# Performance work log

Measured on AMD Instinct MI355X. Metric: run time of the kernel, lower is better.

Reference implementation:

```python
import jax, jax.numpy as jnp
import numpy as np

N = 100000   # nodes
E = 1000000  # edges
IN, HID, OUT = 128, 64, 64


def setup_inputs() -> dict:
    key = jax.random.key(0)
    ks = jax.random.split(key, 6)
    x = jax.random.normal(ks[0], (N, IN), dtype=jnp.float32)
    edge_index = jax.random.randint(ks[1], (2, E), 0, N, dtype=jnp.int64)
    edge_attr = jax.random.uniform(ks[2], (E,), dtype=jnp.float32)
    # Glorot-style init like PyG GCNConv (weight [in, out], bias zeros)
    W1 = jax.random.normal(ks[3], (IN, HID), dtype=jnp.float32) * (1.0 / np.sqrt(IN))
    b1 = jnp.zeros((HID,), dtype=jnp.float32)
    W2 = jax.random.normal(ks[4], (HID, OUT), dtype=jnp.float32) * (1.0 / np.sqrt(HID))
    b2 = jnp.zeros((OUT,), dtype=jnp.float32)
    return {"x": x, "edge_index": edge_index, "edge_attr": edge_attr,
            "W1": W1, "b1": b1, "W2": W2, "b2": b2}


def gcn_conv(x, edge_index, edge_weight, W, b):
    """GCNConv: add self-loops, symmetric normalization, linear + scatter-add."""
    n = x.shape[0]
    row, col = edge_index[0], edge_index[1]
    loop = jnp.arange(n, dtype=row.dtype)
    row = jnp.concatenate([row, loop])
    col = jnp.concatenate([col, loop])
    w = jnp.concatenate([edge_weight, jnp.ones((n,), dtype=x.dtype)])
    deg = jax.ops.segment_sum(w, col, num_segments=n)              # [N]
    dinv = jnp.where(deg > 0, jax.lax.rsqrt(deg), 0.0)
    norm = dinv[row] * w * dinv[col]                               # [E+N]
    h = x @ W                                                      # [N, out]
    agg = jax.ops.segment_sum(h[row] * norm[:, None], col, num_segments=n)
    return agg + b


def reference(x, edge_index, edge_attr, W1, b1, W2, b2):
    h = jax.nn.relu(gcn_conv(x, edge_index, edge_attr, W1, b1))
    return jax.nn.relu(gcn_conv(h, edge_index, edge_attr, W2, b2))
```

## Files before the change

### kernel.cpp

```cpp
#include <hip/hip_runtime.h>


#define BNODES 128
#define LB 7
#define MAXBKT 1024
#define EPT 16
#define EPB (256 * EPT)

typedef __attribute__((ext_vector_type(8))) short bf16x8;
typedef __attribute__((ext_vector_type(4))) float f32x4;

__device__ __forceinline__ unsigned short f2bf(float f) {
    unsigned u = __float_as_uint(f);
    u = (u + 0x7FFF + ((u >> 16) & 1)) >> 16;
    return (unsigned short)u;
}
__device__ __forceinline__ float bf2f(unsigned short h) {
    return __uint_as_float(((unsigned)h) << 16);
}

__device__ __forceinline__ int waveIncScan(int v, int lane) {
    #pragma unroll
    for (int d = 1; d < 64; d <<= 1) {
        int u = __shfl_up(v, d, 64);
        if (lane >= d) v += u;
    }
    return v;
}

__device__ __forceinline__ int blockIncScan(int v, int t, int* wt) {
    int lane = t & 63, w = t >> 6;
    int s = waveIncScan(v, lane);
    if (lane == 63) wt[w] = s;
    __syncthreads();
    int add = 0;
    #pragma unroll
    for (int i = 0; i < 3; ++i) if (i < w) add += wt[i];
    return s + add;
}

__device__ __forceinline__ float4 gather2(
    const unsigned short* __restrict__ G, const int2* __restrict__ eb,
    int m, int p, float4 a0)
{
    float4 a1 = make_float4(0.f, 0.f, 0.f, 0.f);
    int j = 0;
    for (; j + 1 < m; j += 2) {
        int2 pk0 = eb[j];
        int2 pk1 = eb[j + 1];
        float w0 = __int_as_float(pk0.y);
        float w1 = __int_as_float(pk1.y);
        ushort4 g0 = *(const ushort4*)&G[(size_t)pk0.x * 64 + p * 4];
        ushort4 g1 = *(const ushort4*)&G[(size_t)pk1.x * 64 + p * 4];
        a0.x = fmaf(w0, bf2f(g0.x), a0.x); a0.y = fmaf(w0, bf2f(g0.y), a0.y);
        a0.z = fmaf(w0, bf2f(g0.z), a0.z); a0.w = fmaf(w0, bf2f(g0.w), a0.w);
        a1.x = fmaf(w1, bf2f(g1.x), a1.x); a1.y = fmaf(w1, bf2f(g1.y), a1.y);
        a1.z = fmaf(w1, bf2f(g1.z), a1.z); a1.w = fmaf(w1, bf2f(g1.w), a1.w);
    }
    if (j < m) {
        int2 pk = eb[j];
        float w = __int_as_float(pk.y);
        ushort4 g = *(const ushort4*)&G[(size_t)pk.x * 64 + p * 4];
        a0.x = fmaf(w, bf2f(g.x), a0.x); a0.y = fmaf(w, bf2f(g.y), a0.y);
        a0.z = fmaf(w, bf2f(g.z), a0.z); a0.w = fmaf(w, bf2f(g.w), a0.w);
    }
    a0.x += a1.x; a0.y += a1.y; a0.z += a1.z; a0.w += a1.w;
    return a0;
}


__global__ __launch_bounds__(256) void hist_kernel(
    const int* __restrict__ col, int* __restrict__ H, int E, int NBKT,
    const float* __restrict__ W1, const float* __restrict__ W2,
    unsigned short* __restrict__ WT1, unsigned short* __restrict__ WT2, int NEB)
{
    int t = threadIdx.x, blk = blockIdx.x;
    if (blk >= NEB) {
        int i = (blk - NEB) * 256 + t;
        if (i < 64 * 128) {
            int c = i >> 7, k = i & 127;
            WT1[i] = f2bf(W1[k * 64 + c]);
        } else if (i < 64 * 128 + 64 * 64) {
            int j = i - 64 * 128;
            int c = j >> 6, k = j & 63;
            WT2[j] = f2bf(W2[k * 64 + c]);
        }
        return;
    }
    __shared__ int h[MAXBKT];
    for (int b = t; b < NBKT; b += 256) h[b] = 0;
    __syncthreads();
    int base = blk * EPB;
    #pragma unroll
    for (int i = 0; i < EPT; ++i) {
        int e = base + i * 256 + t;
        if (e < E) atomicAdd(&h[col[e] >> LB], 1);
    }
    __syncthreads();
    for (int b = t; b < NBKT; b += 256) H[blk * NBKT + b] = h[b];
}

__global__ __launch_bounds__(256) void rowscan_kernel(
    int* __restrict__ H, int* __restrict__ rowSum, int NEB, int NBKT)
{
    __shared__ int wt[4];
    int b = blockIdx.x, t = threadIdx.x;
    int v = (t < NEB) ? H[t * NBKT + b] : 0;
    int incl = blockIncScan(v, t, wt);
    if (t < NEB) H[t * NBKT + b] = incl - v;
    if (t == 255) rowSum[b] = incl;
}

__global__ __launch_bounds__(256) void bktscan_kernel(
    const int* __restrict__ rowSum, int* __restrict__ bktStart, int NBKT)
{
    __shared__ int wt[4];
    int t = threadIdx.x;
    int v[4]; int sum = 0;
    #pragma unroll
    for (int k = 0; k < 4; ++k) {
        int i = t * 4 + k;
        v[k] = (i < NBKT) ? rowSum[i] : 0;
        sum += v[k];
    }
    int incl = blockIncScan(sum, t, wt);
    int excl = incl - sum;
    #pragma unroll
    for (int k = 0; k < 4; ++k) {
        int i = t * 4 + k;
        if (i < NBKT) bktStart[i] = excl;
        excl += v[k];
    }
    if (t == 255) bktStart[NBKT] = incl;
}

__global__ __launch_bounds__(256) void scatter_gemm_kernel(
    const int* __restrict__ row, const int* __restrict__ col,
    const float* __restrict__ w, const int* __restrict__ H,
    const int* __restrict__ bktStart, int2* __restrict__ sedge1,
    int E, int NBKT, int NEB,
    const float* __restrict__ X, const unsigned short* __restrict__ WT,
    unsigned short* __restrict__ G, int n)
{
    __shared__ char smem[64 * 256 * 2];
    const int t = threadIdx.x;
    const int blk = blockIdx.x;

    if (blk < NEB) {
        int* cur = (int*)smem;
        for (int b = t; b < NBKT; b += 256) cur[b] = bktStart[b] + H[blk * NBKT + b];
        __syncthreads();
        int base = blk * EPB;
        #pragma unroll
        for (int i = 0; i < EPT; ++i) {
            int e = base + i * 256 + t;
            if (e < E) {
                int c = col[e];
                int b = c >> LB;
                int pos = atomicAdd(&cur[b], 1);
                int2 pk;
                pk.x = row[e] | ((c & (BNODES - 1)) << 20);
                pk.y = __float_as_int(w[e]);
                sedge1[pos] = pk;
            }
        }
        return;
    }

    constexpr int K = 128, ROWB = 256, SLOTS = 16, CPR = 32;
    char* xs = smem;
    char* ws = smem + 64 * ROWB;
    const int nodeBase = (blk - NEB) * 64;

    for (int q = t; q < 64 * SLOTS; q += 256) {
        int r = q / SLOTS, s = q % SLOTS;
        uint4 v = *(const uint4*)(WT + r * K + s * 8);
        *(uint4*)(ws + r * ROWB + ((s ^ (r & 7)) * 16)) = v;
    }
    for (int q = t; q < 64 * CPR; q += 256) {
        int r = q / CPR, c = q % CPR;
        int node = nodeBase + r;
        float4 v = make_float4(0.f, 0.f, 0.f, 0.f);
        if (node < n) v = *(const float4*)(X + (size_t)node * K + c * 4);
        ushort4 h;
        h.x = f2bf(v.x); h.y = f2bf(v.y); h.z = f2bf(v.z); h.w = f2bf(v.w);
        *(ushort4*)(xs + r * ROWB + (((c >> 1) ^ (r & 7)) * 16) + (c & 1) * 8) = h;
    }
    __syncthreads();

    const int lane = t & 63;
    const int wv = t >> 6;
    const int lr = lane & 15;
    const int lk = lane >> 4;
    const int arow = (wv << 4) + lr;

    f32x4 acc[4] = {};
    #pragma unroll
    for (int kb = 0; kb < 4; ++kb) {
        int s = kb * 4 + lk;
        bf16x8 a = *(bf16x8*)(xs + arow * ROWB + ((s ^ (arow & 7)) * 16));
        #pragma unroll
        for (int cb = 0; cb < 4; ++cb) {
            int c = cb * 16 + lr;
            bf16x8 b = *(bf16x8*)(ws + c * ROWB + ((s ^ (c & 7)) * 16));
            acc[cb] = __builtin_amdgcn_mfma_f32_16x16x32_bf16(a, b, acc[cb], 0, 0, 0);
        }
    }

    int rowbase = nodeBase + (wv << 4) + (lk << 2);
    #pragma unroll
    for (int j = 0; j < 4; ++j) {
        int node = rowbase + j;
        if (node >= n) continue;
        #pragma unroll
        for (int cb = 0; cb < 4; ++cb)
            G[(size_t)node * 64 + cb * 16 + lr] = f2bf(acc[cb][j]);
    }
}

__global__ __launch_bounds__(256) void fine_kernel(
    const int2* __restrict__ sedge1, const int* __restrict__ bktStart,
    int2* __restrict__ sedge2, int* __restrict__ nodeStart,
    int* __restrict__ nodeCnt, float* __restrict__ dinv,
    unsigned short* __restrict__ g1, int n)
{
    __shared__ int cnt[BNODES];
    __shared__ float wsum[BNODES];
    __shared__ int off[BNODES];
    __shared__ int cur[BNODES];
    __shared__ float dloc[BNODES];
    __shared__ int wt[4];
    int b = blockIdx.x, t = threadIdx.x;
    if (t < BNODES) { cnt[t] = 0; wsum[t] = 1.0f; }
    __syncthreads();
    int s = bktStart[b], e = bktStart[b + 1];
    for (int j = s + t; j < e; j += 256) {
        int2 pk = sedge1[j];
        int ld = pk.x >> 20;
        atomicAdd(&cnt[ld], 1);
        atomicAdd(&wsum[ld], __int_as_float(pk.y));
    }
    __syncthreads();
    int v = (t < BNODES) ? cnt[t] : 0;
    int incl = blockIncScan(v, t, wt);
    if (t < BNODES) {
        off[t] = s + incl - v;
        cur[t] = s + incl - v;
        dloc[t] = rsqrtf(wsum[t]);
    }
    __syncthreads();
    int node = b * BNODES + t;
    if (t < BNODES && node < n) {
        nodeStart[node] = off[t];
        nodeCnt[node] = cnt[t];
        dinv[node] = dloc[t];
    }
    for (int j = s + t; j < e; j += 256) {
        int2 pk = sedge1[j];
        int ld = pk.x >> 20;
        int pos = atomicAdd(&cur[ld], 1);
        sedge2[pos] = make_int2(pk.x & 0xFFFFF, pk.y);
    }
    for (int q = t; q < BNODES * 8; q += 256) {
        int r = q >> 3, cc = q & 7;
        int nd = b * BNODES + r;
        if (nd >= n) continue;
        float dv = dloc[r];
        size_t offb = (size_t)nd * 64 + cc * 8;
        ushort4 u0 = *(const ushort4*)(g1 + offb);
        ushort4 u1 = *(const ushort4*)(g1 + offb + 4);
        u0.x = f2bf(bf2f(u0.x) * dv); u0.y = f2bf(bf2f(u0.y) * dv);
        u0.z = f2bf(bf2f(u0.z) * dv); u0.w = f2bf(bf2f(u0.w) * dv);
        u1.x = f2bf(bf2f(u1.x) * dv); u1.y = f2bf(bf2f(u1.y) * dv);
        u1.z = f2bf(bf2f(u1.z) * dv); u1.w = f2bf(bf2f(u1.w) * dv);
        *(ushort4*)(g1 + offb) = u0;
        *(ushort4*)(g1 + offb + 4) = u1;
    }
}

__global__ __launch_bounds__(256) void aggmm_kernel(
    const unsigned short* __restrict__ G1, const int2* __restrict__ sedge2,
    const int* __restrict__ nodeStart, const int* __restrict__ nodeCnt,
    const float* __restrict__ dinv, const float* __restrict__ bias,
    const unsigned short* __restrict__ WT2, unsigned short* __restrict__ G2, int n)
{
    constexpr int BN = 32;
    constexpr int ROWB = 128;
    __shared__ char smem[(BN + 64) * ROWB];
    char* xs = smem;
    char* ws = smem + BN * ROWB;
    const int tid = threadIdx.x;
    const int nodeBase = blockIdx.x * BN;

    for (int q = tid; q < 64 * 8; q += 256) {
        int r = q >> 3, s = q & 7;
        uint4 v = *(const uint4*)(WT2 + r * 64 + s * 8);
        *(uint4*)(ws + r * ROWB + ((s ^ (r & 7)) * 16)) = v;
    }

    int p = tid & 15;
    float4 bb = *(const float4*)&bias[p * 4];
    #pragma unroll
    for (int pass = 0; pass < 2; ++pass) {
        int r = pass * 16 + (tid >> 4);
        int node = nodeBase + r;
        float4 o = make_float4(0.f, 0.f, 0.f, 0.f);
        if (node < n) {
            ushort4 sv = *(const ushort4*)&G1[(size_t)node * 64 + p * 4];
            float4 a = make_float4(bf2f(sv.x), bf2f(sv.y), bf2f(sv.z), bf2f(sv.w));
            a = gather2(G1, sedge2 + nodeStart[node], nodeCnt[node], p, a);
            float di = dinv[node];
            o.x = fmaxf(fmaf(di, a.x, bb.x), 0.f);
            o.y = fmaxf(fmaf(di, a.y, bb.y), 0.f);
            o.z = fmaxf(fmaf(di, a.z, bb.z), 0.f);
            o.w = fmaxf(fmaf(di, a.w, bb.w), 0.f);
        }
        ushort4 h;
        h.x = f2bf(o.x); h.y = f2bf(o.y); h.z = f2bf(o.z); h.w = f2bf(o.w);
        *(ushort4*)(xs + r * ROWB + (((p >> 1) ^ (r & 7)) * 16) + (p & 1) * 8) = h;
    }
    __syncthreads();

    const int lane = tid & 63;
    const int w = tid >> 6;
    const int lr = lane & 15;
    const int lk = lane >> 4;
    const int rb = w >> 1;
    const int arow = rb * 16 + lr;

    f32x4 acc[2] = {};
    #pragma unroll
    for (int kb = 0; kb < 2; ++kb) {
        int s = kb * 4 + lk;
        bf16x8 a = *(bf16x8*)(xs + arow * ROWB + ((s ^ (arow & 7)) * 16));
        #pragma unroll
        for (int cc = 0; cc < 2; ++cc) {
            int c = ((w & 1) * 2 + cc) * 16 + lr;
            bf16x8 b = *(bf16x8*)(ws + c * ROWB + ((s ^ (c & 7)) * 16));
            acc[cc] = __builtin_amdgcn_mfma_f32_16x16x32_bf16(a, b, acc[cc], 0, 0, 0);
        }
    }

    int rowbase = nodeBase + rb * 16 + (lk << 2);
    #pragma unroll
    for (int j = 0; j < 4; ++j) {
        int node = rowbase + j;
        if (node >= n) continue;
        float dv = dinv[node];
        #pragma unroll
        for (int cc = 0; cc < 2; ++cc)
            G2[(size_t)node * 64 + ((w & 1) * 2 + cc) * 16 + lr] = f2bf(acc[cc][j] * dv);
    }
}

__global__ __launch_bounds__(256) void agg_kernel(
    const unsigned short* __restrict__ G, const int2* __restrict__ sedge2,
    const int* __restrict__ nodeStart, const int* __restrict__ nodeCnt,
    const float* __restrict__ dinv, const float* __restrict__ bias,
    float* __restrict__ OUT, int n)
{
    int t = blockIdx.x * blockDim.x + threadIdx.x;
    if (t >= n * 16) return;
    int node = t >> 4, p = t & 15;

    ushort4 sv = *(const ushort4*)&G[(size_t)node * 64 + p * 4];
    float4 a = make_float4(bf2f(sv.x), bf2f(sv.y), bf2f(sv.z), bf2f(sv.w));
    a = gather2(G, sedge2 + nodeStart[node], nodeCnt[node], p, a);

    float di = dinv[node];
    float4 bb = *(const float4*)&bias[p * 4];
    float4 o;
    o.x = fmaxf(fmaf(di, a.x, bb.x), 0.f);
    o.y = fmaxf(fmaf(di, a.y, bb.y), 0.f);
    o.z = fmaxf(fmaf(di, a.z, bb.z), 0.f);
    o.w = fmaxf(fmaf(di, a.w, bb.w), 0.f);
    *(float4*)&OUT[(size_t)node * 64 + p * 4] = o;
}

extern "C" void kernel_launch(void* const* d_in, const int* in_sizes, int n_in,
                              void* d_out, int out_size, void* d_ws, size_t ws_size,
                              hipStream_t stream) {
    const float* x     = (const float*)d_in[0];
    const int*   eidx  = (const int*)d_in[1];
    const float* eattr = (const float*)d_in[2];
    const float* W1    = (const float*)d_in[3];
    const float* b1    = (const float*)d_in[4];
    const float* W2    = (const float*)d_in[5];
    const float* b2    = (const float*)d_in[6];
    float* out = (float*)d_out;

    const int n = in_sizes[0] / 128;
    const int E = in_sizes[2];
    const int* row = eidx;
    const int* col = eidx + E;

    const int NBKT = (n + BNODES - 1) / BNODES;
    const int NEB  = (E + EPB - 1) / EPB;

    int2*  sedge1 = (int2*)d_ws;
    int2*  sedge2 = sedge1 + (size_t)E;
    unsigned short* g1 = (unsigned short*)(sedge2 + (size_t)E);
    unsigned short* g2 = g1 + (size_t)n * 64;
    unsigned short* WT1 = g2 + (size_t)n * 64;
    unsigned short* WT2 = WT1 + 64 * 128;
    float* dinv      = (float*)(WT2 + 64 * 64);
    int*   nodeStart = (int*)(dinv + n);
    int*   nodeCnt   = nodeStart + n;
    int*   H         = nodeCnt + n;
    int*   rowSum    = H + (size_t)NEB * NBKT;
    int*   bktStart  = rowSum + NBKT;

    const int nbG  = (n + 63) / 64;
    const int nbG2 = (n + 31) / 32;
    const int nbA  = (int)(((size_t)n * 16 + 255) / 256);

    hist_kernel<<<NEB + 48, 256, 0, stream>>>(col, H, E, NBKT, W1, W2, WT1, WT2, NEB);
    rowscan_kernel<<<NBKT, 256, 0, stream>>>(H, rowSum, NEB, NBKT);
    bktscan_kernel<<<1, 256, 0, stream>>>(rowSum, bktStart, NBKT);
    scatter_gemm_kernel<<<NEB + nbG, 256, 0, stream>>>(
        row, col, eattr, H, bktStart, sedge1, E, NBKT, NEB, x, WT1, g1, n);
    fine_kernel<<<NBKT, 256, 0, stream>>>(sedge1, bktStart, sedge2, nodeStart,
                                          nodeCnt, dinv, g1, n);

    aggmm_kernel<<<nbG2, 256, 0, stream>>>(g1, sedge2, nodeStart, nodeCnt, dinv, b1, WT2, g2, n);
    agg_kernel<<<nbA, 256, 0, stream>>>(g2, sedge2, nodeStart, nodeCnt, dinv, b2, out, n);
}
```

Baseline: 126.4 us.

## Coarsen buckets to 512 nodes and stage scatter through LDS for coalesced writes

Raises the coarse bucket width from 128 to 512 nodes, so there are about 196 buckets instead of 782. The scatter blocks now do a local histogram and scan, stage edges in LDS sorted by bucket, and then write them to sedge1 in contiguous runs instead of scattering with per-edge global positions. The fine kernel moves to 512 threads, one per node in a bucket. This cuts scattered global writes and shortens the scans, at the cost of an extra pass over col in each scatter block, a larger LDS footprint, and fewer, heavier fine blocks.

```diff
diff --git a/kernel.cpp b/kernel.cpp
--- a/kernel.cpp
+++ b/kernel.cpp
@@ -1,9 +1,9 @@
 #include <hip/hip_runtime.h>
 
 
-#define BNODES 128
-#define LB 7
-#define MAXBKT 1024
+#define BNODES 512
+#define LB 9
+#define MAXBKT 256
 #define EPT 16
 #define EPB (256 * EPT)
 
@@ -28,6 +28,7 @@
     return v;
 }
 
+template<int NW>
 __device__ __forceinline__ int blockIncScan(int v, int t, int* wt) {
     int lane = t & 63, w = t >> 6;
     int s = waveIncScan(v, lane);
@@ -35,7 +36,7 @@
     __syncthreads();
     int add = 0;
     #pragma unroll
-    for (int i = 0; i < 3; ++i) if (i < w) add += wt[i];
+    for (int i = 0; i < NW - 1; ++i) if (i < w) add += wt[i];
     return s + add;
 }
 
@@ -106,7 +107,7 @@
     __shared__ int wt[4];
     int b = blockIdx.x, t = threadIdx.x;
     int v = (t < NEB) ? H[t * NBKT + b] : 0;
-    int incl = blockIncScan(v, t, wt);
+    int incl = blockIncScan<4>(v, t, wt);
     if (t < NEB) H[t * NBKT + b] = incl - v;
     if (t == 255) rowSum[b] = incl;
 }
@@ -116,24 +117,13 @@
 {
     __shared__ int wt[4];
     int t = threadIdx.x;
-    int v[4]; int sum = 0;
-    #pragma unroll
-    for (int k = 0; k < 4; ++k) {
-        int i = t * 4 + k;
-        v[k] = (i < NBKT) ? rowSum[i] : 0;
-        sum += v[k];
-    }
-    int incl = blockIncScan(sum, t, wt);
-    int excl = incl - sum;
-    #pragma unroll
-    for (int k = 0; k < 4; ++k) {
-        int i = t * 4 + k;
-        if (i < NBKT) bktStart[i] = excl;
-        excl += v[k];
-    }
-    if (t == 255) bktStart[NBKT] = incl;
-}
-
+    int v = (t < NBKT) ? rowSum[t] : 0;
+    int incl = blockIncScan<4>(v, t, wt);
+    if (t < NBKT) bktStart[t] = incl - v;
+    if (t == NBKT - 1) bktStart[NBKT] = incl;
+}
+
+#define SMEMSZ (EPB * 8 + EPB + MAXBKT * 16 + 32)
 __global__ __launch_bounds__(256) void scatter_gemm_kernel(
     const int* __restrict__ row, const int* __restrict__ col,
     const float* __restrict__ w, const int* __restrict__ H,
@@ -142,27 +132,57 @@
     const float* __restrict__ X, const unsigned short* __restrict__ WT,
     unsigned short* __restrict__ G, int n)
 {
-    __shared__ char smem[64 * 256 * 2];
+    __shared__ __align__(16) char smem[SMEMSZ];
     const int t = threadIdx.x;
     const int blk = blockIdx.x;
 
     if (blk < NEB) {
-        int* cur = (int*)smem;
-        for (int b = t; b < NBKT; b += 256) cur[b] = bktStart[b] + H[blk * NBKT + b];
+        int2* stage = (int2*)smem;
+        unsigned char* bstage = (unsigned char*)(stage + EPB);
+        int* lcnt  = (int*)(bstage + EPB);
+        int* loff  = lcnt + MAXBKT;
+        int* lcur  = loff + MAXBKT;
+        int* gbase = lcur + MAXBKT;
+        int* wt    = gbase + MAXBKT;
+
+        for (int b = t; b < NBKT; b += 256) lcnt[b] = 0;
         __syncthreads();
         int base = blk * EPB;
+        #pragma unroll
+        for (int i = 0; i < EPT; ++i) {
+            int e = base + i * 256 + t;
+            if (e < E) atomicAdd(&lcnt[col[e] >> LB], 1);
+        }
+        __syncthreads();
+        int v = (t < NBKT) ? lcnt[t] : 0;
+        int incl = blockIncScan<4>(v, t, wt);
+        if (t < NBKT) {
+            int x0 = incl - v;
+            loff[t] = x0;
+            lcur[t] = x0;
+            gbase[t] = bktStart[t] + H[blk * NBKT + t];
+        }
+        __syncthreads();
         #pragma unroll
         for (int i = 0; i < EPT; ++i) {
             int e = base + i * 256 + t;
             if (e < E) {
                 int c = col[e];
                 int b = c >> LB;
-                int pos = atomicAdd(&cur[b], 1);
+                int pos = atomicAdd(&lcur[b], 1);
                 int2 pk;
                 pk.x = row[e] | ((c & (BNODES - 1)) << 20);
                 pk.y = __float_as_int(w[e]);
-                sedge1[pos] = pk;
+                stage[pos] = pk;
+                bstage[pos] = (unsigned char)b;
             }
+        }
+        __syncthreads();
+        int ecnt = E - base; if (ecnt > EPB) ecnt = EPB;
+        for (int i = t; i < ecnt; i += 256) {
+            int b = bstage[i];
+            int g = gbase[b] + (i - loff[b]);
+            sedge1[g] = stage[i];
         }
         return;
     }
@@ -218,7 +238,7 @@
     }
 }
 
-__global__ __launch_bounds__(256) void fine_kernel(
+__global__ __launch_bounds__(512) void fine_kernel(
     const int2* __restrict__ sedge1, const int* __restrict__ bktStart,
     int2* __restrict__ sedge2, int* __restrict__ nodeStart,
     int* __restrict__ nodeCnt, float* __restrict__ dinv,
@@ -229,39 +249,38 @@
     __shared__ int off[BNODES];
     __shared__ int cur[BNODES];
     __shared__ float dloc[BNODES];
-    __shared__ int wt[4];
+    __shared__ int wt[8];
     int b = blockIdx.x, t = threadIdx.x;
-    if (t < BNODES) { cnt[t] = 0; wsum[t] = 1.0f; }
+    cnt[t] = 0; wsum[t] = 1.0f;
     __syncthreads();
     int s = bktStart[b], e = bktStart[b + 1];
-    for (int j = s + t; j < e; j += 256) {
+    for (int j = s + t; j < e; j += 512) {
         int2 pk = sedge1[j];
         int ld = pk.x >> 20;
         atomicAdd(&cnt[ld], 1);
         atomicAdd(&wsum[ld], __int_as_float(pk.y));
     }
     __syncthreads();
-    int v = (t < BNODES) ? cnt[t] : 0;
-    int incl = blockIncScan(v, t, wt);
-    if (t < BNODES) {
-        off[t] = s + incl - v;
-        cur[t] = s + incl - v;
-        dloc[t] = rsqrtf(wsum[t]);
-    }
+    int v = cnt[t];
+    int incl = blockIncScan<8>(v, t, wt);
+    int x0 = s + incl - v;
+    off[t] = x0;
+    cur[t] = x0;
+    dloc[t] = rsqrtf(wsum[t]);
     __syncthreads();
     int node = b * BNODES + t;
-    if (t < BNODES && node < n) {
+    if (node < n) {
         nodeStart[node] = off[t];
         nodeCnt[node] = cnt[t];
         dinv[node] = dloc[t];
     }
-    for (int j = s + t; j < e; j += 256) {
+    for (int j = s + t; j < e; j += 512) {
         int2 pk = sedge1[j];
         int ld = pk.x >> 20;
         int pos = atomicAdd(&cur[ld], 1);
         sedge2[pos] = make_int2(pk.x & 0xFFFFF, pk.y);
     }
-    for (int q = t; q < BNODES * 8; q += 256) {
+    for (int q = t; q < BNODES * 8; q += 512) {
         int r = q >> 3, cc = q & 7;
         int nd = b * BNODES + r;
         if (nd >= n) continue;
@@ -419,7 +438,7 @@
     bktscan_kernel<<<1, 256, 0, stream>>>(rowSum, bktStart, NBKT);
     scatter_gemm_kernel<<<NEB + nbG, 256, 0, stream>>>(
         row, col, eattr, H, bktStart, sedge1, E, NBKT, NEB, x, WT1, g1, n);
-    fine_kernel<<<NBKT, 256, 0, stream>>>(sedge1, bktStart, sedge2, nodeStart,
+    fine_kernel<<<NBKT, 512, 0, stream>>>(sedge1, bktStart, sedge2, nodeStart,
                                           nodeCnt, dinv, g1, n);
 
     aggmm_kernel<<<nbG2, 256, 0, stream>>>(g1, sedge2, nodeStart, nodeCnt, dinv, b1, WT2, g2, n);
```

After: 122.9 us. -2.7%, faster.
